# Optimization experiments

Hardware: AMD Instinct MI355X
Metric: run time of the kernel (lower is better)

Reference implementation:

```python
import jax, jax.numpy as jnp
import numpy as np

# dims
B, L, T, D = 8, 27, 256, 1152
GS = 3            # group_size
G = L // GS       # num_groups = 9
DD = 512          # downsample_dim
H, HD = 8, 64     # heads, head_dim
NQ = 1            # num_queries
OD = 2048         # output_dim
SCALE = 1.0 / float(np.sqrt(HD))


def setup_inputs() -> dict:
    key = jax.random.key(0)
    ks = jax.random.split(key, 12)
    s = 0.02
    return {
        "K": jax.random.normal(ks[0], (B, L, T, D), jnp.float32),
        "V": jax.random.normal(ks[1], (B, L, T, D), jnp.float32),
        # learnable queries: one (NQ, D) per layer, stacked -> (L, NQ, D)
        "query": jax.random.normal(ks[2], (L, NQ, D), jnp.float32),
        # per-group linear params (flax Linear: y = x @ W + b, W is (in, out))
        "Wq": jax.random.normal(ks[3], (G, D, DD), jnp.float32) * s,
        "bq": jnp.zeros((G, DD), jnp.float32),
        "Wk": jax.random.normal(ks[4], (G, D, DD), jnp.float32) * s,
        "bk": jnp.zeros((G, DD), jnp.float32),
        "Wv": jax.random.normal(ks[5], (G, D, DD), jnp.float32) * s,
        "bv": jnp.zeros((G, DD), jnp.float32),
        "Wo": jax.random.normal(ks[6], (G, DD, OD), jnp.float32) * s,
        "bo": jnp.zeros((G, OD), jnp.float32),
    }


def reference(K, V, query, Wq, bq, Wk, bk, Wv, bv, Wo, bo):
    # group the L layer axis: (B, G, GS, T, D); layers in a group share weights
    Kg = K.reshape(B, G, GS, T, D)
    Vg = V.reshape(B, G, GS, T, D)
    qg = query.reshape(G, GS, NQ, D)

    # projections (batched over groups; replaces L tiny per-layer linears)
    Qp = jnp.einsum('gsnd,gdf->gsnf', qg, Wq) + bq[:, None, None, :]
    Qp = Qp.reshape(G, GS, NQ, H, HD)
    Kp = (jnp.einsum('bgstd,gdf->bgstf', Kg, Wk)
          + bk[None, :, None, None, :]).reshape(B, G, GS, T, H, HD)
    Vp = (jnp.einsum('bgstd,gdf->bgstf', Vg, Wv)
          + bv[None, :, None, None, :]).reshape(B, G, GS, T, H, HD)

    # cross-attention: learnable query attends over T tokens per layer
    scores = jnp.einsum('gsnhe,bgsthe->bgsnht', Qp, Kp) * SCALE
    attn = jax.nn.softmax(scores, axis=-1)
    pooled = jnp.einsum('bgsnht,bgsthe->bgsnhe', attn, Vp)
    pooled = pooled.mean(axis=3)  # mean over queries (== squeeze when NQ=1) -> (B,G,GS,H,HD)

    # original does pooled.transpose(0,2,1).reshape(B, DD): head_dim-major flatten
    pooled = pooled.transpose(0, 1, 2, 4, 3).reshape(B, G, GS, DD)

    out = jnp.einsum('bgsf,gfo->bgso', pooled, Wo) + bo[None, :, None, :]
    return out.reshape(B, L, OD)
```

## Files before the change

### kernel.cpp

```cpp
#include <hip/hip_runtime.h>
#include <stdint.h>


__global__ __launch_bounds__(256) void qproj(
    const float* __restrict__ query, const float* __restrict__ Wq,
    const float* __restrict__ bq, float* __restrict__ Qp)
{
  const int l = blockIdx.x, g = l / 3;
  const int fb = blockIdx.y * 64;
  __shared__ float q[1152];
  __shared__ float part[4][64];
  for (int i = threadIdx.x; i < 1152; i += 256) q[i] = query[(size_t)l * 1152 + i];
  __syncthreads();
  const int fi = threadIdx.x & 63;
  const int kq = threadIdx.x >> 6;
  const float* W = Wq + (size_t)g * 1152 * 512 + fb + fi;
  float a0 = 0.f, a1 = 0.f;
  const int d0 = kq * 288;
#pragma unroll 4
  for (int d = d0; d < d0 + 288; d += 2) {
    a0 += q[d]     * W[(size_t)d * 512];
    a1 += q[d + 1] * W[(size_t)(d + 1) * 512];
  }
  part[kq][fi] = a0 + a1;
  __syncthreads();
  if (threadIdx.x < 64) {
    const int f = fb + threadIdx.x;
    float r = part[0][threadIdx.x] + part[1][threadIdx.x]
            + part[2][threadIdx.x] + part[3][threadIdx.x];
    Qp[l * 512 + f] = (r + bq[g * 512 + f]) * 0.125f;
  }
}

__global__ __launch_bounds__(256) void qk_mat(
    const float* __restrict__ Qp, const float* __restrict__ Wk,
    float* __restrict__ Qk)
{
  const int gidx = blockIdx.x * 256 + threadIdx.x;
  const int eg   = gidx & 3;
  const int item = gidx >> 2;
  const int l    = item / 9216;
  const int rem  = item % 9216;
  const int h    = rem / 1152;
  const int d    = rem % 1152;
  const int g    = l / 3;
  const float4* q4 = (const float4*)(Qp + l * 512 + h * 64 + eg * 16);
  const float4* w4 = (const float4*)(Wk + (size_t)g * 1152 * 512 + (size_t)d * 512 + h * 64 + eg * 16);
  float acc = 0.f;
#pragma unroll
  for (int e = 0; e < 4; e++) {
    const float4 a = q4[e], b = w4[e];
    acc += a.x * b.x + a.y * b.y + a.z * b.z + a.w * b.w;
  }
  acc += __shfl_xor(acc, 1, 64);
  acc += __shfl_xor(acc, 2, 64);
  if (eg == 0) Qk[((size_t)l * 1152 + d) * 8 + h] = acc;
}

__global__ __launch_bounds__(256) void score_k(
    const float* __restrict__ K, const float* __restrict__ Qk,
    float* __restrict__ psc)
{
  const int bl = blockIdx.x;
  const int dq = blockIdx.y;
  const int l = bl % 27;
  const int t = threadIdx.x;

  const float4* Kr = (const float4*)(K + ((size_t)bl * 256 + t) * 1152 + dq * 288);
  const float* qk = Qk + ((size_t)l * 1152 + dq * 288) * 8;

  float sc[8] = {0.f, 0.f, 0.f, 0.f, 0.f, 0.f, 0.f, 0.f};
#pragma unroll 2
  for (int i = 0; i < 72; i++) {
    const float4 kv = Kr[i];
    const float* q0 = qk + (i * 4) * 8;
#pragma unroll
    for (int h = 0; h < 8; h++) {
      sc[h] = fmaf(kv.x, q0[h],      sc[h]);
      sc[h] = fmaf(kv.y, q0[8 + h],  sc[h]);
      sc[h] = fmaf(kv.z, q0[16 + h], sc[h]);
      sc[h] = fmaf(kv.w, q0[24 + h], sc[h]);
    }
  }
  float* dst = psc + (((size_t)bl * 4 + dq) * 256 + t) * 8;
#pragma unroll
  for (int h = 0; h < 8; h++) dst[h] = sc[h];
}

__global__ __launch_bounds__(256) void softmax_k(
    const float* __restrict__ psc, float* __restrict__ attn)
{
  const int bl = blockIdx.x;
  const int t = threadIdx.x;
  const int wid = t >> 6, lane = t & 63;
  __shared__ float red[4][8], red2[4][8];

  float sc[8];
#pragma unroll
  for (int h = 0; h < 8; h++) sc[h] = 0.f;
#pragma unroll
  for (int dq = 0; dq < 4; dq++) {
    const float* src = psc + (((size_t)bl * 4 + dq) * 256 + t) * 8;
#pragma unroll
    for (int h = 0; h < 8; h++) sc[h] += src[h];
  }
#pragma unroll
  for (int h = 0; h < 8; h++) {
    float m = sc[h];
#pragma unroll
    for (int o = 1; o < 64; o <<= 1) m = fmaxf(m, __shfl_xor(m, o, 64));
    if (lane == 0) red[wid][h] = m;
  }
  __syncthreads();
  float p[8];
#pragma unroll
  for (int h = 0; h < 8; h++) {
    const float M = fmaxf(fmaxf(red[0][h], red[1][h]), fmaxf(red[2][h], red[3][h]));
    p[h] = __expf(sc[h] - M);
    float s = p[h];
#pragma unroll
    for (int o = 1; o < 64; o <<= 1) s += __shfl_xor(s, o, 64);
    if (lane == 0) red2[wid][h] = s;
  }
  __syncthreads();
  float* dst = attn + ((size_t)bl * 256 + t) * 8;
#pragma unroll
  for (int h = 0; h < 8; h++) {
    const float S = red2[0][h] + red2[1][h] + red2[2][h] + red2[3][h];
    dst[h] = p[h] * (1.0f / S);
  }
}

__global__ __launch_bounds__(384) void va_k(
    const float* __restrict__ V, const float* __restrict__ attn,
    float* __restrict__ VA)
{
  const int bl = blockIdx.x;
  const int dt = blockIdx.y;
  const int d  = dt * 384 + threadIdx.x;

  const float* Vbase = V + (size_t)bl * 256 * 1152 + d;
  const float* ab = attn + (size_t)bl * 256 * 8;

  float acc[8] = {0.f, 0.f, 0.f, 0.f, 0.f, 0.f, 0.f, 0.f};
#pragma unroll 4
  for (int t = 0; t < 256; t++) {
    const float v = Vbase[(size_t)t * 1152];
    const float* av = ab + t * 8;
#pragma unroll
    for (int h = 0; h < 8; h++) acc[h] = fmaf(av[h], v, acc[h]);
  }
  float* dst = VA + (size_t)bl * 8 * 1152 + d;
#pragma unroll
  for (int h = 0; h < 8; h++) dst[(size_t)h * 1152] = acc[h];
}

__global__ __launch_bounds__(512) void pv_mat(
    const float* __restrict__ VA, const float* __restrict__ Wv,
    float* __restrict__ psum)
{
  const int l = blockIdx.x, g = l / 3, h = blockIdx.y, dz = blockIdx.z;
  const int b = threadIdx.x >> 6, lane = threadIdx.x & 63;
  const int bl = b * 27 + l;
  const float* W = Wv + (size_t)g * 1152 * 512 + h * 64 + lane;
  const float* va = VA + ((size_t)bl * 8 + h) * 1152;
  const int d0 = dz * 288;
  float a0 = 0.f, a1 = 0.f, a2 = 0.f, a3 = 0.f;
#pragma unroll 2
  for (int d = d0; d < d0 + 288; d += 4) {
    a0 = fmaf(va[d],     W[(size_t)(d)     * 512], a0);
    a1 = fmaf(va[d + 1], W[(size_t)(d + 1) * 512], a1);
    a2 = fmaf(va[d + 2], W[(size_t)(d + 2) * 512], a2);
    a3 = fmaf(va[d + 3], W[(size_t)(d + 3) * 512], a3);
  }
  psum[((size_t)dz * 216 + bl) * 512 + lane * 8 + h] = (a0 + a1) + (a2 + a3);
}

__global__ __launch_bounds__(256) void out_gemm(
    const float* __restrict__ psum, const float* __restrict__ bv,
    const float* __restrict__ Wo, const float* __restrict__ bo,
    float* __restrict__ out)
{
  const int l = blockIdx.x, g = l / 3;
  const int n = blockIdx.y * 256 + threadIdx.x;
  __shared__ float pl[8][512];
  for (int i = threadIdx.x; i < 4096; i += 256) {
    const int b = i >> 9, f = i & 511;
    const int bl = b * 27 + l;
    const int e = f >> 3, h = f & 7;
    float v = bv[g * 512 + h * 64 + e];
#pragma unroll
    for (int dz = 0; dz < 4; dz++)
      v += psum[((size_t)dz * 216 + bl) * 512 + f];
    pl[b][f] = v;
  }
  __syncthreads();
  const float* W = Wo + (size_t)g * 512 * 2048 + n;
  float acc[8] = {0.f, 0.f, 0.f, 0.f, 0.f, 0.f, 0.f, 0.f};
#pragma unroll 4
  for (int f = 0; f < 512; f++) {
    const float w = W[(size_t)f * 2048];
#pragma unroll
    for (int b = 0; b < 8; b++) acc[b] += pl[b][f] * w;
  }
  const float bb = bo[g * 2048 + n];
#pragma unroll
  for (int b = 0; b < 8; b++)
    out[(size_t)(b * 27 + l) * 2048 + n] = acc[b] + bb;
}

__global__ __launch_bounds__(256) void zfill(float* __restrict__ out, int n) {
  const int i = blockIdx.x * 256 + threadIdx.x;
  if (i < n) out[i] = 0.f;
}

extern "C" void kernel_launch(void* const* d_in, const int* in_sizes, int n_in,
                              void* d_out, int out_size, void* d_ws, size_t ws_size,
                              hipStream_t stream)
{
  float* out = (float*)d_out;

  bool ok = (n_in == 11) && (out_size == 8 * 27 * 2048);
  if (ok) {
    const int expect[11] = {
      8 * 27 * 256 * 1152,
      8 * 27 * 256 * 1152,
      27 * 1 * 1152,
      9 * 1152 * 512,
      9 * 512,
      9 * 1152 * 512,
      9 * 512,
      9 * 1152 * 512,
      9 * 512,
      9 * 512 * 2048,
      9 * 2048
    };
    for (int i = 0; i < 11; i++) ok = ok && (in_sizes[i] == expect[i]);
  }
  const size_t NEED = 19630080;
  ok = ok && (ws_size >= NEED);

  if (!ok) {
    zfill<<<dim3((out_size + 255) / 256), dim3(256), 0, stream>>>(out, out_size);
    return;
  }

  const float* Kin   = (const float*)d_in[0];
  const float* Vin   = (const float*)d_in[1];
  const float* query = (const float*)d_in[2];
  const float* Wq    = (const float*)d_in[3];
  const float* bq    = (const float*)d_in[4];
  const float* Wk    = (const float*)d_in[5];
  const float* Wv    = (const float*)d_in[7];
  const float* bvp   = (const float*)d_in[8];
  const float* Wo    = (const float*)d_in[9];
  const float* bo    = (const float*)d_in[10];

  char* ws = (char*)d_ws;
  float* Qpw   = (float*)(ws);
  float* Qkw   = (float*)(ws + 55296);
  float* pscw  = (float*)(ws + 1050624);
  float* attnw = (float*)(ws + 8128512);
  float* VAw   = (float*)(ws + 9897984);
  float* psumw = (float*)(ws + 17860608);

  qproj    <<<dim3(27, 8),    dim3(256), 0, stream>>>(query, Wq, bq, Qpw);
  qk_mat   <<<dim3(3888),     dim3(256), 0, stream>>>(Qpw, Wk, Qkw);
  score_k  <<<dim3(216, 4),   dim3(256), 0, stream>>>(Kin, Qkw, pscw);
  softmax_k<<<dim3(216),      dim3(256), 0, stream>>>(pscw, attnw);
  va_k     <<<dim3(216, 3),   dim3(384), 0, stream>>>(Vin, attnw, VAw);
  pv_mat   <<<dim3(27, 8, 4), dim3(512), 0, stream>>>(VAw, Wv, psumw);
  out_gemm <<<dim3(27, 8),    dim3(256), 0, stream>>>(psumw, bvp, Wo, bo, out);
}
```

Baseline: 311.9 us.

## Stage K rows through LDS for coalesced score loads and split V by token

score_k now splits the token axis instead of the feature axis. Each block loads 64 K rows into padded shared memory with coalesced float4 reads, then reduces partial head scores in LDS, so softmax reads a single score buffer. va_k now splits over token quarters with float2 loads and 576 threads covering all 1152 features, writing four partial VA buffers. pv_mat sums those partials on the fly. The intent is better coalescing of the dominant K and V streams, at the cost of a larger workspace and extra partial reads.

```diff
diff --git a/kernel.cpp b/kernel.cpp
--- a/kernel.cpp
+++ b/kernel.cpp
@@ -59,36 +59,59 @@
 
 __global__ __launch_bounds__(256) void score_k(
     const float* __restrict__ K, const float* __restrict__ Qk,
-    float* __restrict__ psc)
+    float* __restrict__ scores)
 {
   const int bl = blockIdx.x;
-  const int dq = blockIdx.y;
+  const int tq = blockIdx.y;
   const int l = bl % 27;
-  const int t = threadIdx.x;
-
-  const float4* Kr = (const float4*)(K + ((size_t)bl * 256 + t) * 1152 + dq * 288);
-  const float* qk = Qk + ((size_t)l * 1152 + dq * 288) * 8;
+  const int tid = threadIdx.x;
+  const int tt = tid & 63;
+  const int ds = tid >> 6;
+
+  __shared__ float lds[64 * 195];
+
+  const float* Kbase = K + ((size_t)bl * 256 + tq * 64) * 1152;
+  const float* qkl = Qk + (size_t)l * 1152 * 8;
 
   float sc[8] = {0.f, 0.f, 0.f, 0.f, 0.f, 0.f, 0.f, 0.f};
-#pragma unroll 2
-  for (int i = 0; i < 72; i++) {
-    const float4 kv = Kr[i];
-    const float* q0 = qk + (i * 4) * 8;
-#pragma unroll
-    for (int h = 0; h < 8; h++) {
-      sc[h] = fmaf(kv.x, q0[h],      sc[h]);
-      sc[h] = fmaf(kv.y, q0[8 + h],  sc[h]);
-      sc[h] = fmaf(kv.z, q0[16 + h], sc[h]);
-      sc[h] = fmaf(kv.w, q0[24 + h], sc[h]);
+
+  for (int dc = 0; dc < 6; dc++) {
+    __syncthreads();
+#pragma unroll
+    for (int it = 0; it < 12; it++) {
+      const int flat = it * 256 + tid;
+      const int row = flat / 48, col = flat % 48;
+      const float4 v = *(const float4*)(Kbase + (size_t)row * 1152 + dc * 192 + col * 4);
+      float* p = &lds[row * 195 + col * 4];
+      p[0] = v.x; p[1] = v.y; p[2] = v.z; p[3] = v.w;
     }
-  }
-  float* dst = psc + (((size_t)bl * 4 + dq) * 256 + t) * 8;
-#pragma unroll
-  for (int h = 0; h < 8; h++) dst[h] = sc[h];
+    __syncthreads();
+    const float* q0 = qkl + (size_t)(dc * 192 + ds * 48) * 8;
+    const float* krow = &lds[tt * 195 + ds * 48];
+#pragma unroll 6
+    for (int j = 0; j < 48; j++) {
+      const float kv = krow[j];
+      const float* q = q0 + j * 8;
+#pragma unroll
+      for (int h = 0; h < 8; h++) sc[h] = fmaf(kv, q[h], sc[h]);
+    }
+  }
+
+  __syncthreads();
+#pragma unroll
+  for (int h = 0; h < 8; h++) lds[(ds * 64 + tt) * 8 + h] = sc[h];
+  __syncthreads();
+  if (tid < 64) {
+    float* dst = scores + ((size_t)bl * 256 + tq * 64 + tid) * 8;
+#pragma unroll
+    for (int h = 0; h < 8; h++)
+      dst[h] = (lds[(0 * 64 + tid) * 8 + h] + lds[(1 * 64 + tid) * 8 + h])
+             + (lds[(2 * 64 + tid) * 8 + h] + lds[(3 * 64 + tid) * 8 + h]);
+  }
 }
 
 __global__ __launch_bounds__(256) void softmax_k(
-    const float* __restrict__ psc, float* __restrict__ attn)
+    const float* __restrict__ scores, float* __restrict__ attn)
 {
   const int bl = blockIdx.x;
   const int t = threadIdx.x;
@@ -96,14 +119,9 @@
   __shared__ float red[4][8], red2[4][8];
 
   float sc[8];
-#pragma unroll
-  for (int h = 0; h < 8; h++) sc[h] = 0.f;
-#pragma unroll
-  for (int dq = 0; dq < 4; dq++) {
-    const float* src = psc + (((size_t)bl * 4 + dq) * 256 + t) * 8;
-#pragma unroll
-    for (int h = 0; h < 8; h++) sc[h] += src[h];
-  }
+  const float* src = scores + ((size_t)bl * 256 + t) * 8;
+#pragma unroll
+  for (int h = 0; h < 8; h++) sc[h] = src[h];
 #pragma unroll
   for (int h = 0; h < 8; h++) {
     float m = sc[h];
@@ -131,49 +149,61 @@
   }
 }
 
-__global__ __launch_bounds__(384) void va_k(
+__global__ __launch_bounds__(576) void va_k(
     const float* __restrict__ V, const float* __restrict__ attn,
-    float* __restrict__ VA)
+    float* __restrict__ VAp)
 {
   const int bl = blockIdx.x;
-  const int dt = blockIdx.y;
-  const int d  = dt * 384 + threadIdx.x;
-
-  const float* Vbase = V + (size_t)bl * 256 * 1152 + d;
-  const float* ab = attn + (size_t)bl * 256 * 8;
-
-  float acc[8] = {0.f, 0.f, 0.f, 0.f, 0.f, 0.f, 0.f, 0.f};
+  const int tq = blockIdx.y;
+  const int w = threadIdx.x >> 6, lane = threadIdx.x & 63;
+  const int d = w * 128 + lane * 2;
+
+  const float* Vbase = V + ((size_t)bl * 256 + tq * 64) * 1152 + d;
+  const float* ab = attn + ((size_t)bl * 256 + tq * 64) * 8;
+
+  float2 acc[8];
+#pragma unroll
+  for (int h = 0; h < 8; h++) acc[h] = make_float2(0.f, 0.f);
+
 #pragma unroll 4
-  for (int t = 0; t < 256; t++) {
-    const float v = Vbase[(size_t)t * 1152];
+  for (int t = 0; t < 64; t++) {
+    const float2 v = *(const float2*)(Vbase + (size_t)t * 1152);
     const float* av = ab + t * 8;
 #pragma unroll
-    for (int h = 0; h < 8; h++) acc[h] = fmaf(av[h], v, acc[h]);
-  }
-  float* dst = VA + (size_t)bl * 8 * 1152 + d;
-#pragma unroll
-  for (int h = 0; h < 8; h++) dst[(size_t)h * 1152] = acc[h];
+    for (int h = 0; h < 8; h++) {
+      acc[h].x = fmaf(av[h], v.x, acc[h].x);
+      acc[h].y = fmaf(av[h], v.y, acc[h].y);
+    }
+  }
+  float* dst = VAp + (((size_t)tq * 216 + bl) * 8) * 1152 + d;
+#pragma unroll
+  for (int h = 0; h < 8; h++)
+    *(float2*)(dst + (size_t)h * 1152) = acc[h];
 }
 
 __global__ __launch_bounds__(512) void pv_mat(
-    const float* __restrict__ VA, const float* __restrict__ Wv,
+    const float* __restrict__ VAp, const float* __restrict__ Wv,
     float* __restrict__ psum)
 {
   const int l = blockIdx.x, g = l / 3, h = blockIdx.y, dz = blockIdx.z;
   const int b = threadIdx.x >> 6, lane = threadIdx.x & 63;
   const int bl = b * 27 + l;
   const float* W = Wv + (size_t)g * 1152 * 512 + h * 64 + lane;
-  const float* va = VA + ((size_t)bl * 8 + h) * 1152;
+  const size_t stride = (size_t)216 * 8 * 1152;
+  const float* v0 = VAp + ((size_t)bl * 8 + h) * 1152;
+  const float* v1 = v0 + stride;
+  const float* v2 = v1 + stride;
+  const float* v3 = v2 + stride;
   const int d0 = dz * 288;
-  float a0 = 0.f, a1 = 0.f, a2 = 0.f, a3 = 0.f;
-#pragma unroll 2
-  for (int d = d0; d < d0 + 288; d += 4) {
-    a0 = fmaf(va[d],     W[(size_t)(d)     * 512], a0);
-    a1 = fmaf(va[d + 1], W[(size_t)(d + 1) * 512], a1);
-    a2 = fmaf(va[d + 2], W[(size_t)(d + 2) * 512], a2);
-    a3 = fmaf(va[d + 3], W[(size_t)(d + 3) * 512], a3);
-  }
-  psum[((size_t)dz * 216 + bl) * 512 + lane * 8 + h] = (a0 + a1) + (a2 + a3);
+  float a0 = 0.f, a1 = 0.f;
+#pragma unroll 4
+  for (int d = d0; d < d0 + 288; d += 2) {
+    const float va  = (v0[d]     + v1[d])     + (v2[d]     + v3[d]);
+    const float vb  = (v0[d + 1] + v1[d + 1]) + (v2[d + 1] + v3[d + 1]);
+    a0 = fmaf(va, W[(size_t)d * 512],       a0);
+    a1 = fmaf(vb, W[(size_t)(d + 1) * 512], a1);
+  }
+  psum[((size_t)dz * 216 + bl) * 512 + lane * 8 + h] = a0 + a1;
 }
 
 __global__ __launch_bounds__(256) void out_gemm(
@@ -237,7 +267,7 @@
     };
     for (int i = 0; i < 11; i++) ok = ok && (in_sizes[i] == expect[i]);
   }
-  const size_t NEED = 19630080;
+  const size_t NEED = 38209536;
   ok = ok && (ws_size >= NEED);
 
   if (!ok) {
@@ -257,18 +287,18 @@
   const float* bo    = (const float*)d_in[10];
 
   char* ws = (char*)d_ws;
-  float* Qpw   = (float*)(ws);
-  float* Qkw   = (float*)(ws + 55296);
-  float* pscw  = (float*)(ws + 1050624);
-  float* attnw = (float*)(ws + 8128512);
-  float* VAw   = (float*)(ws + 9897984);
-  float* psumw = (float*)(ws + 17860608);
+  float* Qpw     = (float*)(ws);
+  float* Qkw     = (float*)(ws + 55296);
+  float* scoresw = (float*)(ws + 1050624);
+  float* attnw   = (float*)(ws + 2820096);
+  float* VApw    = (float*)(ws + 4589568);
+  float* psumw   = (float*)(ws + 36440064);
 
   qproj    <<<dim3(27, 8),    dim3(256), 0, stream>>>(query, Wq, bq, Qpw);
   qk_mat   <<<dim3(3888),     dim3(256), 0, stream>>>(Qpw, Wk, Qkw);
-  score_k  <<<dim3(216, 4),   dim3(256), 0, stream>>>(Kin, Qkw, pscw);
-  softmax_k<<<dim3(216),      dim3(256), 0, stream>>>(pscw, attnw);
-  va_k     <<<dim3(216, 3),   dim3(384), 0, stream>>>(Vin, attnw, VAw);
-  pv_mat   <<<dim3(27, 8, 4), dim3(512), 0, stream>>>(VAw, Wv, psumw);
+  score_k  <<<dim3(216, 4),   dim3(256), 0, stream>>>(Kin, Qkw, scoresw);
+  softmax_k<<<dim3(216),      dim3(256), 0, stream>>>(scoresw, attnw);
+  va_k     <<<dim3(216, 4),   dim3(576), 0, stream>>>(Vin, attnw, VApw);
+  pv_mat   <<<dim3(27, 8, 4), dim3(512), 0, stream>>>(VApw, Wv, psumw);
   out_gemm <<<dim3(27, 8),    dim3(256), 0, stream>>>(psumw, bvp, Wo, bo, out);
 }
```

Result: slower. 362.2 us (+16.1%).

## Fuse score and softmax kernels via shared memory; widen va_k to float2 per thread

Applied to the files above, without the earlier changes.

Merges the partial-score kernel and the softmax kernel into one 1024-thread block per (b,l). The four d-quarter partial scores are reduced in shared memory instead of being written to and read back from a global workspace, which removes one launch and the psc round trip. The V-times-attention kernel now uses one 576-thread block per (b,l) with float2 loads and stores covering all 1152 columns, replacing three 384-thread blocks. Only 216 blocks are launched for each of these two kernels, so fewer blocks run concurrently on the GPU, and three quarters of the threads sit idle during the softmax phase.

```diff
diff --git a/kernel.cpp b/kernel.cpp
--- a/kernel.cpp
+++ b/kernel.cpp
@@ -57,102 +57,106 @@
   if (eg == 0) Qk[((size_t)l * 1152 + d) * 8 + h] = acc;
 }
 
-__global__ __launch_bounds__(256) void score_k(
+__global__ __launch_bounds__(1024) void score_sm_k(
     const float* __restrict__ K, const float* __restrict__ Qk,
-    float* __restrict__ psc)
+    float* __restrict__ attn)
 {
   const int bl = blockIdx.x;
-  const int dq = blockIdx.y;
   const int l = bl % 27;
-  const int t = threadIdx.x;
-
-  const float4* Kr = (const float4*)(K + ((size_t)bl * 256 + t) * 1152 + dq * 288);
-  const float* qk = Qk + ((size_t)l * 1152 + dq * 288) * 8;
-
-  float sc[8] = {0.f, 0.f, 0.f, 0.f, 0.f, 0.f, 0.f, 0.f};
+  const int tid = threadIdx.x;
+  const int t  = tid & 255;
+  const int dq = tid >> 8;
+
+  __shared__ float psc[4][256][8];
+  __shared__ float red[4][8], red2[4][8];
+
+  {
+    const float4* Kr = (const float4*)(K + ((size_t)bl * 256 + t) * 1152 + dq * 288);
+    const float* qk = Qk + ((size_t)l * 1152 + dq * 288) * 8;
+    float sc[8] = {0.f, 0.f, 0.f, 0.f, 0.f, 0.f, 0.f, 0.f};
 #pragma unroll 2
-  for (int i = 0; i < 72; i++) {
-    const float4 kv = Kr[i];
-    const float* q0 = qk + (i * 4) * 8;
-#pragma unroll
-    for (int h = 0; h < 8; h++) {
-      sc[h] = fmaf(kv.x, q0[h],      sc[h]);
-      sc[h] = fmaf(kv.y, q0[8 + h],  sc[h]);
-      sc[h] = fmaf(kv.z, q0[16 + h], sc[h]);
-      sc[h] = fmaf(kv.w, q0[24 + h], sc[h]);
-    }
-  }
-  float* dst = psc + (((size_t)bl * 4 + dq) * 256 + t) * 8;
-#pragma unroll
-  for (int h = 0; h < 8; h++) dst[h] = sc[h];
-}
-
-__global__ __launch_bounds__(256) void softmax_k(
-    const float* __restrict__ psc, float* __restrict__ attn)
-{
-  const int bl = blockIdx.x;
-  const int t = threadIdx.x;
-  const int wid = t >> 6, lane = t & 63;
-  __shared__ float red[4][8], red2[4][8];
-
-  float sc[8];
-#pragma unroll
-  for (int h = 0; h < 8; h++) sc[h] = 0.f;
-#pragma unroll
-  for (int dq = 0; dq < 4; dq++) {
-    const float* src = psc + (((size_t)bl * 4 + dq) * 256 + t) * 8;
-#pragma unroll
-    for (int h = 0; h < 8; h++) sc[h] += src[h];
-  }
-#pragma unroll
-  for (int h = 0; h < 8; h++) {
-    float m = sc[h];
-#pragma unroll
-    for (int o = 1; o < 64; o <<= 1) m = fmaxf(m, __shfl_xor(m, o, 64));
-    if (lane == 0) red[wid][h] = m;
-  }
-  __syncthreads();
-  float p[8];
-#pragma unroll
-  for (int h = 0; h < 8; h++) {
-    const float M = fmaxf(fmaxf(red[0][h], red[1][h]), fmaxf(red[2][h], red[3][h]));
-    p[h] = __expf(sc[h] - M);
-    float s = p[h];
-#pragma unroll
-    for (int o = 1; o < 64; o <<= 1) s += __shfl_xor(s, o, 64);
-    if (lane == 0) red2[wid][h] = s;
-  }
-  __syncthreads();
-  float* dst = attn + ((size_t)bl * 256 + t) * 8;
-#pragma unroll
-  for (int h = 0; h < 8; h++) {
-    const float S = red2[0][h] + red2[1][h] + red2[2][h] + red2[3][h];
-    dst[h] = p[h] * (1.0f / S);
-  }
-}
-
-__global__ __launch_bounds__(384) void va_k(
+    for (int i = 0; i < 72; i++) {
+      const float4 kv = Kr[i];
+      const float* q0 = qk + (i * 4) * 8;
+#pragma unroll
+      for (int h = 0; h < 8; h++) {
+        sc[h] = fmaf(kv.x, q0[h],      sc[h]);
+        sc[h] = fmaf(kv.y, q0[8 + h],  sc[h]);
+        sc[h] = fmaf(kv.z, q0[16 + h], sc[h]);
+        sc[h] = fmaf(kv.w, q0[24 + h], sc[h]);
+      }
+    }
+#pragma unroll
+    for (int h = 0; h < 8; h++) psc[dq][t][h] = sc[h];
+  }
+  __syncthreads();
+
+  const int wid = tid >> 6, lane = tid & 63;
+  float sc[8], p[8];
+  if (tid < 256) {
+#pragma unroll
+    for (int h = 0; h < 8; h++)
+      sc[h] = (psc[0][tid][h] + psc[1][tid][h]) + (psc[2][tid][h] + psc[3][tid][h]);
+#pragma unroll
+    for (int h = 0; h < 8; h++) {
+      float m = sc[h];
+#pragma unroll
+      for (int o = 1; o < 64; o <<= 1) m = fmaxf(m, __shfl_xor(m, o, 64));
+      if (lane == 0) red[wid][h] = m;
+    }
+  }
+  __syncthreads();
+  if (tid < 256) {
+#pragma unroll
+    for (int h = 0; h < 8; h++) {
+      const float M = fmaxf(fmaxf(red[0][h], red[1][h]), fmaxf(red[2][h], red[3][h]));
+      p[h] = __expf(sc[h] - M);
+      float s = p[h];
+#pragma unroll
+      for (int o = 1; o < 64; o <<= 1) s += __shfl_xor(s, o, 64);
+      if (lane == 0) red2[wid][h] = s;
+    }
+  }
+  __syncthreads();
+  if (tid < 256) {
+    float* dst = attn + ((size_t)bl * 256 + tid) * 8;
+#pragma unroll
+    for (int h = 0; h < 8; h++) {
+      const float S = red2[0][h] + red2[1][h] + red2[2][h] + red2[3][h];
+      dst[h] = p[h] * (1.0f / S);
+    }
+  }
+}
+
+__global__ __launch_bounds__(576) void va_k(
     const float* __restrict__ V, const float* __restrict__ attn,
     float* __restrict__ VA)
 {
   const int bl = blockIdx.x;
-  const int dt = blockIdx.y;
-  const int d  = dt * 384 + threadIdx.x;
+  const int w = threadIdx.x >> 6, lane = threadIdx.x & 63;
+  const int d = w * 128 + lane * 2;
 
   const float* Vbase = V + (size_t)bl * 256 * 1152 + d;
   const float* ab = attn + (size_t)bl * 256 * 8;
 
-  float acc[8] = {0.f, 0.f, 0.f, 0.f, 0.f, 0.f, 0.f, 0.f};
+  float2 acc[8];
+#pragma unroll
+  for (int h = 0; h < 8; h++) acc[h] = make_float2(0.f, 0.f);
+
 #pragma unroll 4
   for (int t = 0; t < 256; t++) {
-    const float v = Vbase[(size_t)t * 1152];
+    const float2 v = *(const float2*)(Vbase + (size_t)t * 1152);
     const float* av = ab + t * 8;
 #pragma unroll
-    for (int h = 0; h < 8; h++) acc[h] = fmaf(av[h], v, acc[h]);
+    for (int h = 0; h < 8; h++) {
+      acc[h].x = fmaf(av[h], v.x, acc[h].x);
+      acc[h].y = fmaf(av[h], v.y, acc[h].y);
+    }
   }
   float* dst = VA + (size_t)bl * 8 * 1152 + d;
 #pragma unroll
-  for (int h = 0; h < 8; h++) dst[(size_t)h * 1152] = acc[h];
+  for (int h = 0; h < 8; h++)
+    *(float2*)(dst + (size_t)h * 1152) = acc[h];
 }
 
 __global__ __launch_bounds__(512) void pv_mat(
@@ -237,7 +241,7 @@
     };
     for (int i = 0; i < 11; i++) ok = ok && (in_sizes[i] == expect[i]);
   }
-  const size_t NEED = 19630080;
+  const size_t NEED = 12552192;
   ok = ok && (ws_size >= NEED);
 
   if (!ok) {
@@ -259,16 +263,14 @@
   char* ws = (char*)d_ws;
   float* Qpw   = (float*)(ws);
   float* Qkw   = (float*)(ws + 55296);
-  float* pscw  = (float*)(ws + 1050624);
-  float* attnw = (float*)(ws + 8128512);
-  float* VAw   = (float*)(ws + 9897984);
-  float* psumw = (float*)(ws + 17860608);
-
-  qproj    <<<dim3(27, 8),    dim3(256), 0, stream>>>(query, Wq, bq, Qpw);
-  qk_mat   <<<dim3(3888),     dim3(256), 0, stream>>>(Qpw, Wk, Qkw);
-  score_k  <<<dim3(216, 4),   dim3(256), 0, stream>>>(Kin, Qkw, pscw);
-  softmax_k<<<dim3(216),      dim3(256), 0, stream>>>(pscw, attnw);
-  va_k     <<<dim3(216, 3),   dim3(384), 0, stream>>>(Vin, attnw, VAw);
-  pv_mat   <<<dim3(27, 8, 4), dim3(512), 0, stream>>>(VAw, Wv, psumw);
-  out_gemm <<<dim3(27, 8),    dim3(256), 0, stream>>>(psumw, bvp, Wo, bo, out);
-}
+  float* attnw = (float*)(ws + 1050624);
+  float* VAw   = (float*)(ws + 2820096);
+  float* psumw = (float*)(ws + 10782720);
+
+  qproj     <<<dim3(27, 8),    dim3(256),  0, stream>>>(query, Wq, bq, Qpw);
+  qk_mat    <<<dim3(3888),     dim3(256),  0, stream>>>(Qpw, Wk, Qkw);
+  score_sm_k<<<dim3(216),      dim3(1024), 0, stream>>>(Kin, Qkw, attnw);
+  va_k      <<<dim3(216),      dim3(576),  0, stream>>>(Vin, attnw, VAw);
+  pv_mat    <<<dim3(27, 8, 4), dim3(512),  0, stream>>>(VAw, Wv, psumw);
+  out_gemm  <<<dim3(27, 8),    dim3(256),  0, stream>>>(psumw, bvp, Wo, bo, out);
+}
```

After: 344.6 us. 1.1x slower.
